# Kernel tuning notes

Measured on AMD Instinct MI355X. Metric: run time of the kernel, lower is better.

## Reference

```python
import jax, jax.numpy as jnp
import numpy as np

TEMP = 0.07
EPS = 1e-12


def _l2norm(x):
    # F.normalize(x, dim=1): divide by clamped L2 norm
    n = jnp.sqrt(jnp.sum(x * x, axis=1, keepdims=True))
    return x / jnp.maximum(n, EPS)


def _pool_cat(slow, fast):
    # AdaptiveAvgPool3d((1,1,1)) == mean over (T,H,W); concat channels -> [B, 2304]
    return jnp.concatenate([slow.mean(axis=(2, 3, 4)), fast.mean(axis=(2, 3, 4))], axis=1)


def _sim_targets(sim_labels, same_idx):
    # Vectorized replacement of the per-row python loop; targets are constants
    # (built from .item() in torch), hence stop_gradient.
    B = sim_labels.shape[0]
    eye = jnp.eye(B, dtype=sim_labels.dtype)
    pos = jnp.diagonal(sim_labels)[:, None]                    # [B,1]
    neg = (1.0 - pos) / (B - 1)
    soft = eye * pos + (1.0 - eye) * neg                       # same_idx in {1,3,4}
    uni = jnp.full((B, B), 1.0 / B, dtype=sim_labels.dtype)    # same_idx == 0
    si = same_idx[:, None]
    t = jnp.where(si == 2, eye, jnp.where(si == 0, uni, soft))
    return jax.lax.stop_gradient(t)


def setup_inputs() -> dict:
    key = jax.random.key(0)
    ks = jax.random.split(key, 16)
    B = 64
    inp = {
        "fpv_slow": jax.random.normal(ks[0], (B, 2048, 8, 7, 7), jnp.float32),
        "fpv_fast": jax.random.normal(ks[1], (B, 256, 32, 7, 7), jnp.float32),
        "tpv_slow": jax.random.normal(ks[2], (B, 2048, 8, 7, 7), jnp.float32),
        "tpv_fast": jax.random.normal(ks[3], (B, 256, 32, 7, 7), jnp.float32),
        "labels_v": jax.random.uniform(ks[4], (B, 97), jnp.float32),
        "labels_n": jax.random.uniform(ks[5], (B, 300), jnp.float32),
        "labels_v_lt": jax.random.uniform(ks[6], (B, 97), jnp.float32),
        "labels_n_lt": jax.random.uniform(ks[7], (B, 300), jnp.float32),
        "same_idx": jax.random.randint(ks[8], (B,), 0, 5, jnp.int64 if jax.config.jax_enable_x64 else jnp.int32),
        "W_fpv": jax.random.normal(ks[9], (2304, 256), jnp.float32) * 0.02,
        "b_fpv": jax.random.normal(ks[10], (256,), jnp.float32) * 0.02,
        "W_tpv": jax.random.normal(ks[11], (2304, 256), jnp.float32) * 0.02,
        "b_tpv": jax.random.normal(ks[12], (256,), jnp.float32) * 0.02,
    }
    return inp


def reference(fpv_slow, fpv_fast, tpv_slow, tpv_fast,
              labels_v, labels_n, labels_v_lt, labels_n_lt,
              same_idx, W_fpv, b_fpv, W_tpv, b_tpv):
    x_fpv = _l2norm(_pool_cat(fpv_slow, fpv_fast))             # [B,2304]
    x_tpv = _l2norm(_pool_cat(tpv_slow, tpv_fast))
    f = _l2norm(x_fpv @ W_fpv + b_fpv)                         # [B,256]
    t = _l2norm(x_tpv @ W_tpv + b_tpv)
    sim_preds = (f @ t.T) / TEMP                               # [B,B]
    sim_labels = (labels_v @ labels_v_lt.T + labels_n @ labels_n_lt.T) * 0.5
    targets = _sim_targets(sim_labels, same_idx)
    loss = -jnp.sum(jax.nn.log_softmax(sim_preds, axis=1) * targets, axis=1).mean()
    return loss
```

## Files before the change

kernel.cpp:

```cpp
#include <hip/hip_runtime.h>
#include <math.h>

#define TEMP 0.07f
#define EPSN 1e-12f

__device__ __forceinline__ float wave_reduce_sum(float v) {
    #pragma unroll
    for (int off = 32; off > 0; off >>= 1)
        v += __shfl_xor(v, off, 64);
    return v;
}

__device__ __forceinline__ float wave_reduce_max(float v) {
    #pragma unroll
    for (int off = 32; off > 0; off >>= 1)
        v = fmaxf(v, __shfl_xor(v, off, 64));
    return v;
}

__global__ __launch_bounds__(256) void pool_kernel(
    const float* __restrict__ fpv_slow, const float* __restrict__ fpv_fast,
    const float* __restrict__ tpv_slow, const float* __restrict__ tpv_fast,
    float* __restrict__ pool )
{
    const int gw   = (int)((blockIdx.x * blockDim.x + threadIdx.x) >> 6);
    const int lane = threadIdx.x & 63;

    if (gw < 65536) {
        const int tensor = gw >> 15;
        const int base   = (gw & 32767) * 4;
        const float* src = tensor ? tpv_slow : fpv_slow;
        const float4* p  = (const float4*)src;
        const bool lo    = lane < 34;

        const float4 a0 = p[(size_t)(base + 0) * 98 + lane];
        const float4 a1 = p[(size_t)(base + 1) * 98 + lane];
        const float4 a2 = p[(size_t)(base + 2) * 98 + lane];
        const float4 a3 = p[(size_t)(base + 3) * 98 + lane];
        float s0 = a0.x + a0.y + a0.z + a0.w;
        float s1 = a1.x + a1.y + a1.z + a1.w;
        float s2 = a2.x + a2.y + a2.z + a2.w;
        float s3 = a3.x + a3.y + a3.z + a3.w;
        if (lo) {
            const float4 b0 = p[(size_t)(base + 0) * 98 + 64 + lane];
            const float4 b1 = p[(size_t)(base + 1) * 98 + 64 + lane];
            const float4 b2 = p[(size_t)(base + 2) * 98 + 64 + lane];
            const float4 b3 = p[(size_t)(base + 3) * 98 + 64 + lane];
            s0 += b0.x + b0.y + b0.z + b0.w;
            s1 += b1.x + b1.y + b1.z + b1.w;
            s2 += b2.x + b2.y + b2.z + b2.w;
            s3 += b3.x + b3.y + b3.z + b3.w;
        }
        s0 = wave_reduce_sum(s0);
        s1 = wave_reduce_sum(s1);
        s2 = wave_reduce_sum(s2);
        s3 = wave_reduce_sum(s3);
        if (lane == 0) {
            const int b = base >> 11, c = base & 2047;
            float4 o = make_float4(s0, s1, s2, s3);
            o.x *= (1.0f / 392.0f); o.y *= (1.0f / 392.0f);
            o.z *= (1.0f / 392.0f); o.w *= (1.0f / 392.0f);
            *(float4*)&pool[tensor * (64 * 2304) + b * 2304 + c] = o;
        }
    } else {
        const int w2     = gw - 65536;
        const int tensor = w2 >> 14;
        const int row    = w2 & 16383;
        const float* src = tensor ? tpv_fast : fpv_fast;
        const float4* p  = (const float4*)src + (size_t)row * 392;
        const float4 a0 = p[lane];
        const float4 a1 = p[64 + lane];
        const float4 a2 = p[128 + lane];
        const float4 a3 = p[192 + lane];
        const float4 a4 = p[256 + lane];
        const float4 a5 = p[320 + lane];
        float s = (a0.x + a0.y + a0.z + a0.w) + (a1.x + a1.y + a1.z + a1.w)
                + (a2.x + a2.y + a2.z + a2.w) + (a3.x + a3.y + a3.z + a3.w)
                + (a4.x + a4.y + a4.z + a4.w) + (a5.x + a5.y + a5.z + a5.w);
        if (lane < 8) {
            const float4 t = p[384 + lane];
            s += t.x + t.y + t.z + t.w;
        }
        s = wave_reduce_sum(s);
        if (lane == 0) {
            const int b = row >> 8, c = row & 255;
            pool[tensor * (64 * 2304) + b * 2304 + 2048 + c] = s * (1.0f / 1568.0f);
        }
    }
}

__global__ __launch_bounds__(256) void gemv_kernel(
    const float* __restrict__ pool,
    const float* __restrict__ W_f, const float* __restrict__ W_t,
    float* __restrict__ gp )
{
    __shared__ float xs[256];
    __shared__ float partial[4][256];

    const int tid = threadIdx.x, wv = tid >> 6, lane = tid & 63;
    const int idx = blockIdx.x;
    const int ks  = idx % 9;
    const int hb  = idx / 9;
    const int h   = hb >> 6, b = hb & 63;
    const float* W = h ? W_t : W_f;

    xs[tid] = pool[h * (64 * 2304) + b * 2304 + ks * 256 + tid];
    __syncthreads();

    float4 acc = make_float4(0.f, 0.f, 0.f, 0.f);
    const float4* Wv = (const float4*)W + (size_t)(ks * 256 + wv * 64) * 64 + lane;
    #pragma unroll 8
    for (int kk = 0; kk < 64; ++kk) {
        const float xk = xs[wv * 64 + kk];
        const float4 w4 = Wv[(size_t)kk * 64];
        acc.x += xk * w4.x; acc.y += xk * w4.y;
        acc.z += xk * w4.z; acc.w += xk * w4.w;
    }
    *(float4*)&partial[wv][4 * lane] = acc;
    __syncthreads();

    gp[(size_t)idx * 256 + tid] =
        partial[0][tid] + partial[1][tid] + partial[2][tid] + partial[3][tid];
}

__global__ __launch_bounds__(256) void finalize_kernel(
    const float* __restrict__ pool, const float* __restrict__ gp,
    const float* __restrict__ b_f, const float* __restrict__ b_t,
    float* __restrict__ ft )
{
    __shared__ float red[8];
    const int tid = threadIdx.x, wv = tid >> 6, lane = tid & 63;
    const int h = blockIdx.x >> 6, b = blockIdx.x & 63;

    const float* xrow = pool + h * (64 * 2304) + b * 2304;
    float ss = 0.0f;
    #pragma unroll
    for (int r = 0; r < 9; ++r) {
        const float v = xrow[tid + r * 256];
        ss += v * v;
    }
    ss = wave_reduce_sum(ss);
    if (lane == 0) red[wv] = ss;
    __syncthreads();
    const float scale1 = 1.0f / fmaxf(sqrtf(red[0] + red[1] + red[2] + red[3]), EPSN);

    float y = 0.0f;
    const float* g = gp + (size_t)(h * 64 + b) * 9 * 256;
    #pragma unroll
    for (int ks = 0; ks < 9; ++ks) y += g[ks * 256 + tid];
    const float* bias = h ? b_t : b_f;
    y = y * scale1 + bias[tid];

    const float ss2 = wave_reduce_sum(y * y);
    if (lane == 0) red[4 + wv] = ss2;
    __syncthreads();
    const float scale2 = 1.0f / fmaxf(sqrtf(red[4] + red[5] + red[6] + red[7]), EPSN);

    ft[h * (64 * 256) + b * 256 + tid] = y * scale2;
}

__global__ __launch_bounds__(256) void loss_kernel(
    const float* __restrict__ ft,
    const float* __restrict__ lv, const float* __restrict__ lvlt,
    const float* __restrict__ ln, const float* __restrict__ lnlt,
    const int* __restrict__ same_idx,
    float* __restrict__ out)
{
    __shared__ float fs[256];
    __shared__ float sim[64];
    __shared__ float pos_sh;

    const int i   = blockIdx.x;
    const int tid = threadIdx.x, wv = tid >> 6, lane = tid & 63;
    const float* f = ft;
    const float* t = ft + 64 * 256;

    fs[tid] = f[i * 256 + tid];
    if (wv == 3) {
        float s = 0.0f;
        for (int k = lane; k < 97; k += 64)  s += lv[i * 97 + k]  * lvlt[i * 97 + k];
        for (int k = lane; k < 300; k += 64) s += ln[i * 300 + k] * lnlt[i * 300 + k];
        s = wave_reduce_sum(s);
        if (lane == 0) pos_sh = 0.5f * s;
    }
    __syncthreads();

    const float4 a = ((const float4*)fs)[lane];
    for (int jj = 0; jj < 16; ++jj) {
        const int j = wv * 16 + jj;
        const float4 b4 = ((const float4*)(t + j * 256))[lane];
        float d = a.x * b4.x + a.y * b4.y + a.z * b4.z + a.w * b4.w;
        d = wave_reduce_sum(d);
        if (lane == 0) sim[j] = d / TEMP;
    }
    __syncthreads();

    if (wv == 0) {
        const int si = same_idx[i];
        const float pos = pos_sh;
        const float x = sim[lane];
        const float m = wave_reduce_max(x);
        const float e = expf(x - m);
        const float s = wave_reduce_sum(e);
        const float lse = logf(s);
        float w;
        if (si == 2)      w = (lane == i) ? 1.0f : 0.0f;
        else if (si == 0) w = 1.0f / 64.0f;
        else {
            const float neg = (1.0f - pos) * (1.0f / 63.0f);
            w = (lane == i) ? pos : neg;
        }
        const float dotv = wave_reduce_sum(w * x);
        if (lane == 0) atomicAdd(out, (m + lse - dotv) * (1.0f / 64.0f));
    }
}

extern "C" void kernel_launch(void* const* d_in, const int* in_sizes, int n_in,
                              void* d_out, int out_size, void* d_ws, size_t ws_size,
                              hipStream_t stream) {
    const float* fpv_slow   = (const float*)d_in[0];
    const float* fpv_fast   = (const float*)d_in[1];
    const float* tpv_slow   = (const float*)d_in[2];
    const float* tpv_fast   = (const float*)d_in[3];
    const float* labels_v    = (const float*)d_in[4];
    const float* labels_n    = (const float*)d_in[5];
    const float* labels_v_lt = (const float*)d_in[6];
    const float* labels_n_lt = (const float*)d_in[7];
    const int*   same_idx    = (const int*)d_in[8];
    const float* W_fpv = (const float*)d_in[9];
    const float* b_fpv = (const float*)d_in[10];
    const float* W_tpv = (const float*)d_in[11];
    const float* b_tpv = (const float*)d_in[12];

    float* pool = (float*)d_ws;
    float* gp   = pool + 2 * 64 * 2304;
    float* ft   = gp + 1152 * 256;
    float* out  = (float*)d_out;

    hipMemsetAsync(d_out, 0, sizeof(float) * out_size, stream);

    pool_kernel<<<24576, 256, 0, stream>>>(fpv_slow, fpv_fast, tpv_slow, tpv_fast, pool);
    gemv_kernel<<<1152, 256, 0, stream>>>(pool, W_fpv, W_tpv, gp);
    finalize_kernel<<<128, 256, 0, stream>>>(pool, gp, b_fpv, b_tpv, ft);
    loss_kernel<<<64, 256, 0, stream>>>(ft, labels_v, labels_v_lt, labels_n, labels_n_lt,
                                        same_idx, out);
}
```

Before: 558.7 us.

## Make pooling kernel persistent with double-buffered register prefetch

```diff
diff --git a/kernel.cpp b/kernel.cpp
--- a/kernel.cpp
+++ b/kernel.cpp
@@ -23,69 +23,102 @@
     const float* __restrict__ tpv_slow, const float* __restrict__ tpv_fast,
     float* __restrict__ pool )
 {
-    const int gw   = (int)((blockIdx.x * blockDim.x + threadIdx.x) >> 6);
-    const int lane = threadIdx.x & 63;
-
-    if (gw < 65536) {
-        const int tensor = gw >> 15;
-        const int base   = (gw & 32767) * 4;
-        const float* src = tensor ? tpv_slow : fpv_slow;
-        const float4* p  = (const float4*)src;
-        const bool lo    = lane < 34;
-
-        const float4 a0 = p[(size_t)(base + 0) * 98 + lane];
-        const float4 a1 = p[(size_t)(base + 1) * 98 + lane];
-        const float4 a2 = p[(size_t)(base + 2) * 98 + lane];
-        const float4 a3 = p[(size_t)(base + 3) * 98 + lane];
-        float s0 = a0.x + a0.y + a0.z + a0.w;
-        float s1 = a1.x + a1.y + a1.z + a1.w;
-        float s2 = a2.x + a2.y + a2.z + a2.w;
-        float s3 = a3.x + a3.y + a3.z + a3.w;
-        if (lo) {
-            const float4 b0 = p[(size_t)(base + 0) * 98 + 64 + lane];
-            const float4 b1 = p[(size_t)(base + 1) * 98 + 64 + lane];
-            const float4 b2 = p[(size_t)(base + 2) * 98 + 64 + lane];
-            const float4 b3 = p[(size_t)(base + 3) * 98 + 64 + lane];
-            s0 += b0.x + b0.y + b0.z + b0.w;
-            s1 += b1.x + b1.y + b1.z + b1.w;
-            s2 += b2.x + b2.y + b2.z + b2.w;
-            s3 += b3.x + b3.y + b3.z + b3.w;
+    const int wv   = (int)(threadIdx.x >> 6);
+    const int lane = (int)(threadIdx.x & 63);
+    const int gw   = (int)blockIdx.x * 4 + wv;
+    const float4 z4 = make_float4(0.f, 0.f, 0.f, 0.f);
+
+    if (gw < 2048) {
+        const float4* pf = (const float4*)fpv_slow;
+        const float4* pt = (const float4*)tpv_slow;
+        const bool lo = lane < 34;
+        float4 xa0,xa1,xa2,xa3,xb0,xb1,xb2,xb3;
+        float4 ya0,ya1,ya2,ya3,yb0,yb1,yb2,yb3;
+
+#define SLOAD(U,A0,A1,A2,A3,B0,B1,B2,B3)  do {                                \
+        const int u_ = (U);                                                   \
+        const float4* q_ = ((u_ < 32768) ? pf : pt)                           \
+                           + (size_t)(u_ & 32767) * 392 + lane;               \
+        A0 = q_[0]; A1 = q_[98]; A2 = q_[196]; A3 = q_[294];                  \
+        B0 = z4; B1 = z4; B2 = z4; B3 = z4;                                   \
+        if (lo) { B0 = q_[64]; B1 = q_[162]; B2 = q_[260]; B3 = q_[358]; }    \
+    } while (0)
+
+#define SRED(U,A0,A1,A2,A3,B0,B1,B2,B3)  do {                                 \
+        const int u_ = (U);                                                   \
+        float s0 = (A0.x+A0.y+A0.z+A0.w) + (B0.x+B0.y+B0.z+B0.w);             \
+        float s1 = (A1.x+A1.y+A1.z+A1.w) + (B1.x+B1.y+B1.z+B1.w);             \
+        float s2 = (A2.x+A2.y+A2.z+A2.w) + (B2.x+B2.y+B2.z+B2.w);             \
+        float s3 = (A3.x+A3.y+A3.z+A3.w) + (B3.x+B3.y+B3.z+B3.w);             \
+        s0 = wave_reduce_sum(s0); s1 = wave_reduce_sum(s1);                   \
+        s2 = wave_reduce_sum(s2); s3 = wave_reduce_sum(s3);                   \
+        if (lane == 0) {                                                      \
+            const int tn_ = u_ >> 15, rb_ = (u_ & 32767) * 4;                 \
+            const int b_ = rb_ >> 11, c_ = rb_ & 2047;                        \
+            float4 o;                                                         \
+            o.x = s0*(1.0f/392.0f); o.y = s1*(1.0f/392.0f);                   \
+            o.z = s2*(1.0f/392.0f); o.w = s3*(1.0f/392.0f);                   \
+            *(float4*)&pool[tn_ * (64*2304) + b_ * 2304 + c_] = o;            \
+        }                                                                     \
+    } while (0)
+
+        SLOAD(gw, xa0,xa1,xa2,xa3,xb0,xb1,xb2,xb3);
+        #pragma unroll 1
+        for (int it = 0; it < 30; it += 2) {
+            SLOAD(gw + (it+1)*2048, ya0,ya1,ya2,ya3,yb0,yb1,yb2,yb3);
+            SRED (gw + it*2048,     xa0,xa1,xa2,xa3,xb0,xb1,xb2,xb3);
+            SLOAD(gw + (it+2)*2048, xa0,xa1,xa2,xa3,xb0,xb1,xb2,xb3);
+            SRED (gw + (it+1)*2048, ya0,ya1,ya2,ya3,yb0,yb1,yb2,yb3);
         }
-        s0 = wave_reduce_sum(s0);
-        s1 = wave_reduce_sum(s1);
-        s2 = wave_reduce_sum(s2);
-        s3 = wave_reduce_sum(s3);
-        if (lane == 0) {
-            const int b = base >> 11, c = base & 2047;
-            float4 o = make_float4(s0, s1, s2, s3);
-            o.x *= (1.0f / 392.0f); o.y *= (1.0f / 392.0f);
-            o.z *= (1.0f / 392.0f); o.w *= (1.0f / 392.0f);
-            *(float4*)&pool[tensor * (64 * 2304) + b * 2304 + c] = o;
+        SLOAD(gw + 31*2048, ya0,ya1,ya2,ya3,yb0,yb1,yb2,yb3);
+        SRED (gw + 30*2048, xa0,xa1,xa2,xa3,xb0,xb1,xb2,xb3);
+        SRED (gw + 31*2048, ya0,ya1,ya2,ya3,yb0,yb1,yb2,yb3);
+#undef SLOAD
+#undef SRED
+    } else {
+        const int fw = gw - 2048;
+        const float4* pf = (const float4*)fpv_fast;
+        const float4* pt = (const float4*)tpv_fast;
+        const bool t8 = lane < 8;
+        float4 xa0,xa1,xa2,xa3,xa4,xa5,xt;
+        float4 ya0,ya1,ya2,ya3,ya4,ya5,yt;
+
+#define FLOAD(U,A0,A1,A2,A3,A4,A5,T)  do {                                    \
+        const int u_ = (U);                                                   \
+        const float4* q_ = ((u_ < 16384) ? pf : pt)                           \
+                           + (size_t)(u_ & 16383) * 392 + lane;               \
+        A0 = q_[0];   A1 = q_[64];  A2 = q_[128];                             \
+        A3 = q_[192]; A4 = q_[256]; A5 = q_[320];                             \
+        T = z4; if (t8) T = q_[384];                                          \
+    } while (0)
+
+#define FRED(U,A0,A1,A2,A3,A4,A5,T)  do {                                     \
+        const int u_ = (U);                                                   \
+        float s = (A0.x+A0.y+A0.z+A0.w) + (A1.x+A1.y+A1.z+A1.w)               \
+                + (A2.x+A2.y+A2.z+A2.w) + (A3.x+A3.y+A3.z+A3.w)               \
+                + (A4.x+A4.y+A4.z+A4.w) + (A5.x+A5.y+A5.z+A5.w)               \
+                + (T.x+T.y+T.z+T.w);                                          \
+        s = wave_reduce_sum(s);                                               \
+        if (lane == 0) {                                                      \
+            const int tn_ = u_ >> 14, row_ = u_ & 16383;                      \
+            pool[tn_ * (64*2304) + (row_ >> 8) * 2304 + 2048 + (row_ & 255)]  \
+                = s * (1.0f/1568.0f);                                         \
+        }                                                                     \
+    } while (0)
+
+        FLOAD(fw, xa0,xa1,xa2,xa3,xa4,xa5,xt);
+        #pragma unroll 1
+        for (int it = 0; it < 30; it += 2) {
+            FLOAD(fw + (it+1)*1024, ya0,ya1,ya2,ya3,ya4,ya5,yt);
+            FRED (fw + it*1024,     xa0,xa1,xa2,xa3,xa4,xa5,xt);
+            FLOAD(fw + (it+2)*1024, xa0,xa1,xa2,xa3,xa4,xa5,xt);
+            FRED (fw + (it+1)*1024, ya0,ya1,ya2,ya3,ya4,ya5,yt);
         }
-    } else {
-        const int w2     = gw - 65536;
-        const int tensor = w2 >> 14;
-        const int row    = w2 & 16383;
-        const float* src = tensor ? tpv_fast : fpv_fast;
-        const float4* p  = (const float4*)src + (size_t)row * 392;
-        const float4 a0 = p[lane];
-        const float4 a1 = p[64 + lane];
-        const float4 a2 = p[128 + lane];
-        const float4 a3 = p[192 + lane];
-        const float4 a4 = p[256 + lane];
-        const float4 a5 = p[320 + lane];
-        float s = (a0.x + a0.y + a0.z + a0.w) + (a1.x + a1.y + a1.z + a1.w)
-                + (a2.x + a2.y + a2.z + a2.w) + (a3.x + a3.y + a3.z + a3.w)
-                + (a4.x + a4.y + a4.z + a4.w) + (a5.x + a5.y + a5.z + a5.w);
-        if (lane < 8) {
-            const float4 t = p[384 + lane];
-            s += t.x + t.y + t.z + t.w;
-        }
-        s = wave_reduce_sum(s);
-        if (lane == 0) {
-            const int b = row >> 8, c = row & 255;
-            pool[tensor * (64 * 2304) + b * 2304 + 2048 + c] = s * (1.0f / 1568.0f);
-        }
+        FLOAD(fw + 31*1024, ya0,ya1,ya2,ya3,ya4,ya5,yt);
+        FRED (fw + 30*1024, xa0,xa1,xa2,xa3,xa4,xa5,xt);
+        FRED (fw + 31*1024, ya0,ya1,ya2,ya3,ya4,ya5,yt);
+#undef FLOAD
+#undef FRED
     }
 }
 
@@ -239,7 +272,7 @@
 
     hipMemsetAsync(d_out, 0, sizeof(float) * out_size, stream);
 
-    pool_kernel<<<24576, 256, 0, stream>>>(fpv_slow, fpv_fast, tpv_slow, tpv_fast, pool);
+    pool_kernel<<<768, 256, 0, stream>>>(fpv_slow, fpv_fast, tpv_slow, tpv_fast, pool);
     gemv_kernel<<<1152, 256, 0, stream>>>(pool, W_fpv, W_tpv, gp);
     finalize_kernel<<<128, 256, 0, stream>>>(pool, gp, b_fpv, b_tpv, ft);
     loss_kernel<<<64, 256, 0, stream>>>(ft, labels_v, labels_v_lt, labels_n, labels_n_lt,
```

New measurement: 561.5 us. No clear change (+0.5%).
